# Kernel optimization log

Measured on AMD Instinct MI355X. Metric: run time of the kernel, lower is better.

Reference implementation:

```python
import jax, jax.numpy as jnp
import numpy as np

EMB = 32
B = 2048
L = 375
LAYERS = [512, 256, 128]
PROJ = 5
TABLE_SIZES = {
    'name_table': 1000001, 'collab_table': 3, 'track_uri_can_table': 1000001,
    'n_songs_table': 101, 'n_artists_table': 101, 'n_albums_table': 101,
    'artist_name_table': 300001, 'track_uri_pl_table': 1000001, 'track_name_table': 1000001,
    'duration_table': 101, 'album_name_table': 500001, 'artist_pop_table': 11,
    'followers_table': 11, 'track_pop_table': 11, 'genres_table': 2001,
}
IDX_SPECS = [
    ('name_idx', (B,), 1000001), ('collaborative_idx', (B,), 3), ('track_uri_can_idx', (B,), 1000001),
    ('n_songs_idx', (B,), 101), ('num_artists_idx', (B,), 101), ('num_albums_idx', (B,), 101),
    ('artist_name_pl_idx', (B, L), 300001), ('track_uri_pl_idx', (B, L), 1000001),
    ('track_name_pl_idx', (B, L), 1000001), ('duration_ms_idx', (B, L), 101),
    ('album_name_pl_idx', (B, L), 500001), ('artist_pop_idx', (B, L), 11),
    ('artists_followers_idx', (B, L), 11), ('track_pop_idx', (B, L), 11),
    ('artist_genres_idx', (B, L), 2001),
]


def setup_inputs() -> dict:
    key = jax.random.key(0)
    n_keys = len(IDX_SPECS) + len(TABLE_SIZES) + 10
    keys = iter(jax.random.split(key, n_keys))
    inp = {}
    for name, shape, hi in IDX_SPECS:
        inp[name] = jax.random.randint(next(keys), shape, 0, hi, dtype=jnp.int32)
    for name, n in TABLE_SIZES.items():
        inp[name] = jax.random.normal(next(keys), (n, EMB), jnp.float32) * 0.05
    d_in = 15 * EMB  # 480 concatenated features
    inp['cross_V'] = jax.random.normal(next(keys), (d_in, PROJ), jnp.float32) * 0.05
    inp['cross_U'] = jax.random.normal(next(keys), (PROJ, d_in), jnp.float32) * 0.05
    inp['cross_b'] = jnp.zeros((d_in,), jnp.float32)
    dims = [d_in] + LAYERS
    for i in range(3):
        inp[f'W{i+1}'] = jax.random.normal(next(keys), (dims[i], dims[i+1]), jnp.float32) * (1.0 / np.sqrt(dims[i]))
        inp[f'b{i+1}'] = jnp.zeros((dims[i+1],), jnp.float32)
    return inp


def _fwd(idx, tables, cross_V, cross_U, cross_b, W1, b1, W2, b2, W3, b3):
    # scalar features: single-row gather -> [B, EMB]
    # sequence features: gather [B, L, EMB] then mean-pool over L (GlobalAveragePooling1D)
    embs = []
    for ix, tab in zip(idx, tables):
        e = tab[ix]                                  # [B,EMB] or [B,L,EMB]
        if e.ndim == 3:
            e = e.mean(axis=1)                       # avg pool over playlist length
        embs.append(e)
    x0 = jnp.concatenate(embs, axis=1)               # [B, 480]
    # tfrs DCN cross layer (low-rank): x0 * ((x0 @ V) @ U + b) + x0
    proj = (x0 @ cross_V) @ cross_U + cross_b
    x = x0 * proj + x0
    # dense tower: relu, relu, linear, l2-normalize
    x = jax.nn.relu(x @ W1 + b1)
    x = jax.nn.relu(x @ W2 + b2)
    x = x @ W3 + b3
    norm = jnp.sqrt(jnp.maximum(jnp.sum(x * x, axis=1, keepdims=True), 1e-12))
    return x / norm


def reference(name_idx, collaborative_idx, track_uri_can_idx, n_songs_idx, num_artists_idx,
              num_albums_idx, artist_name_pl_idx, track_uri_pl_idx, track_name_pl_idx,
              duration_ms_idx, album_name_pl_idx, artist_pop_idx, artists_followers_idx,
              track_pop_idx, artist_genres_idx, name_table, collab_table, track_uri_can_table,
              n_songs_table, n_artists_table, n_albums_table, artist_name_table,
              track_uri_pl_table, track_name_table, duration_table, album_name_table,
              artist_pop_table, followers_table, track_pop_table, genres_table,
              cross_V, cross_U, cross_b, W1, b1, W2, b2, W3, b3):
    idx = [name_idx, collaborative_idx, track_uri_can_idx, n_songs_idx, num_artists_idx,
           num_albums_idx, artist_name_pl_idx, track_uri_pl_idx, track_name_pl_idx,
           duration_ms_idx, album_name_pl_idx, artist_pop_idx, artists_followers_idx,
           track_pop_idx, artist_genres_idx]
    tables = [name_table, collab_table, track_uri_can_table, n_songs_table, n_artists_table,
              n_albums_table, artist_name_table, track_uri_pl_table, track_name_table,
              duration_table, album_name_table, artist_pop_table, followers_table,
              track_pop_table, genres_table]
    return _fwd(idx, tables, cross_V, cross_U, cross_b, W1, b1, W2, b2, W3, b3)
```

## Files before the change

kernel.cpp:

```cpp
#include <hip/hip_runtime.h>
#include <cmath>

#define NB 2048
#define NL 375
#define NLP 384
#define NEMB 32
#define DIN 480

typedef __attribute__((ext_vector_type(8))) short short8;
typedef __attribute__((ext_vector_type(4))) short short4v;
typedef __attribute__((ext_vector_type(4))) float f32x4;

__device__ inline short f2bf(float x) {
  union { float f; unsigned u; } v; v.f = x;
  unsigned r = v.u + 0x7fffu + ((v.u >> 16) & 1u);
  return (short)(r >> 16);
}

struct SeqArgs {
  const int*   idx[9];
  const float* tab[9];
};

template <bool NT>
__device__ inline float4 gather_pool_body(const float* __restrict__ tab,
                                          const int* __restrict__ sidx,
                                          int s, int c) {
  const f32x4* tab4 = reinterpret_cast<const f32x4*>(tab);
  f32x4 acc = {0.f, 0.f, 0.f, 0.f};
  #pragma unroll
  for (int it = 0; it < 11; ++it) {
    const int l = s + it * 32;
    f32x4 v = NT ? __builtin_nontemporal_load(&tab4[(size_t)sidx[l] * 8 + c])
                 : tab4[(size_t)sidx[l] * 8 + c];
    acc += v;
  }
  {
    const int l = s + 352;
    f32x4 v = NT ? __builtin_nontemporal_load(&tab4[(size_t)sidx[l] * 8 + c])
                 : tab4[(size_t)sidx[l] * 8 + c];
    if (s < 23) acc += v;
  }
  return make_float4(acc.x, acc.y, acc.z, acc.w);
}

__global__ __launch_bounds__(256) void seq_pool_kernel(SeqArgs args, float* __restrict__ x0) {
  const int bid = blockIdx.x;
  const int f   = bid % 9;
  const int b   = bid / 9;
  const int tid = threadIdx.x;

  __shared__ int sidx[NLP];
  const int*   idx = args.idx[f];
  const float* tab = args.tab[f];

  for (int i = tid; i < NLP; i += 256)
    sidx[i] = (i < NL) ? __builtin_nontemporal_load(&idx[b * NL + i])
                       : __builtin_nontemporal_load(&idx[b * NL]);
  __syncthreads();

  const int c = tid & 7;
  const int s = tid >> 3;

  float4 acc = (f == 1 || f == 2) ? gather_pool_body<true>(tab, sidx, s, c)
                                  : gather_pool_body<false>(tab, sidx, s, c);

  #pragma unroll
  for (int off = 8; off <= 32; off <<= 1) {
    acc.x += __shfl_xor(acc.x, off, 64);
    acc.y += __shfl_xor(acc.y, off, 64);
    acc.z += __shfl_xor(acc.z, off, 64);
    acc.w += __shfl_xor(acc.w, off, 64);
  }

  __shared__ float4 wpart[4][8];
  const int wave = tid >> 6;
  const int lane = tid & 63;
  if (lane < 8) wpart[wave][lane] = acc;
  __syncthreads();

  if (tid < 8) {
    float4 s0 = wpart[0][tid], s1 = wpart[1][tid], s2 = wpart[2][tid], s3 = wpart[3][tid];
    const float inv = 1.0f / (float)NL;
    float4 r;
    r.x = (s0.x + s1.x + s2.x + s3.x) * inv;
    r.y = (s0.y + s1.y + s2.y + s3.y) * inv;
    r.z = (s0.z + s1.z + s2.z + s3.z) * inv;
    r.w = (s0.w + s1.w + s2.w + s3.w) * inv;
    float* out = x0 + (size_t)b * DIN + (6 + f) * NEMB + tid * 4;
    *reinterpret_cast<float4*>(out) = r;
  }
}

struct ScalArgs {
  const int*   idx[6];
  const float* tab[6];
};

__global__ __launch_bounds__(64) void cross_scalar_kernel(ScalArgs args,
                                                          const float* __restrict__ x0,
                                                          short* __restrict__ x0b,
                                                          const float* __restrict__ V,
                                                          const float* __restrict__ U,
                                                          const float* __restrict__ bias) {
  const int b    = blockIdx.x;
  const int lane = threadIdx.x;
  const float* row = x0 + (size_t)b * DIN;
  short* rowb = x0b + (size_t)b * DIN;

  float xv[8];
  float t[5] = {0.f, 0.f, 0.f, 0.f, 0.f};
  #pragma unroll
  for (int i = 0; i < 8; ++i) {
    int j = lane + i * 64;
    float x;
    if (i < 3) {
      int f = j >> 5, d = j & 31;
      x = args.tab[f][(size_t)args.idx[f][b] * NEMB + d];
    } else if (j < DIN) {
      x = row[j];
    } else {
      x = 0.f;
    }
    xv[i] = x;
    if (j < DIN) {
      #pragma unroll
      for (int p = 0; p < 5; ++p) t[p] += x * V[j * 5 + p];
    }
  }
  #pragma unroll
  for (int p = 0; p < 5; ++p) {
    float v = t[p];
    for (int off = 32; off; off >>= 1) v += __shfl_xor(v, off, 64);
    t[p] = v;
  }
  #pragma unroll
  for (int i = 0; i < 8; ++i) {
    int j = lane + i * 64;
    if (j < DIN) {
      float proj = bias[j];
      #pragma unroll
      for (int p = 0; p < 5; ++p) proj += t[p] * U[p * DIN + j];
      rowb[j] = f2bf(xv[i] * proj + xv[i]);
    }
  }
}

template <bool RELU>
__global__ __launch_bounds__(256) void gemm_mfma_kernel(const short* __restrict__ A,
                                                        const float* __restrict__ W,
                                                        const float* __restrict__ bias,
                                                        short* __restrict__ C,
                                                        int M, int N, int K) {
  const int tid  = threadIdx.x;
  const int m0   = blockIdx.y * 64;
  const int n0   = blockIdx.x * 64;
  const int wave = tid >> 6;
  const int lane = tid & 63;
  const int wm   = wave >> 1;
  const int wn   = wave & 1;

  __shared__ short As[64][40];
  __shared__ short Bs[64][40];

  f32x4 acc[2][2];
  #pragma unroll
  for (int i = 0; i < 2; ++i)
    #pragma unroll
    for (int j = 0; j < 2; ++j)
      acc[i][j] = (f32x4){0.f, 0.f, 0.f, 0.f};

  const int am  = tid >> 2;
  const int akq = tid & 3;
  const int bn  = tid & 63;
  const int bkg = tid >> 6;

  for (int k0 = 0; k0 < K; k0 += 32) {
    {
      short8 av = *reinterpret_cast<const short8*>(&A[(size_t)(m0 + am) * K + k0 + akq * 8]);
      *reinterpret_cast<short8*>(&As[am][akq * 8]) = av;
    }
    {
      float bv[8];
      #pragma unroll
      for (int i = 0; i < 8; ++i)
        bv[i] = W[(size_t)(k0 + bkg * 8 + i) * N + n0 + bn];
      short8 wv = { f2bf(bv[0]), f2bf(bv[1]), f2bf(bv[2]), f2bf(bv[3]),
                    f2bf(bv[4]), f2bf(bv[5]), f2bf(bv[6]), f2bf(bv[7]) };
      *reinterpret_cast<short8*>(&Bs[bn][bkg * 8]) = wv;
    }
    __syncthreads();

    short8 bf[2];
    #pragma unroll
    for (int fn = 0; fn < 2; ++fn)
      bf[fn] = *reinterpret_cast<const short8*>(&Bs[wn * 32 + fn * 16 + (lane & 15)][(lane >> 4) * 8]);
    #pragma unroll
    for (int fm = 0; fm < 2; ++fm) {
      short8 af = *reinterpret_cast<const short8*>(&As[wm * 32 + fm * 16 + (lane & 15)][(lane >> 4) * 8]);
      #pragma unroll
      for (int fn = 0; fn < 2; ++fn)
        acc[fm][fn] = __builtin_amdgcn_mfma_f32_16x16x32_bf16(af, bf[fn], acc[fm][fn], 0, 0, 0);
    }
    __syncthreads();
  }

  #pragma unroll
  for (int fm = 0; fm < 2; ++fm) {
    #pragma unroll
    for (int fn = 0; fn < 2; ++fn) {
      const int col  = n0 + wn * 32 + fn * 16 + (lane & 15);
      const float bc = bias[col];
      #pragma unroll
      for (int r = 0; r < 4; ++r) {
        const int m = m0 + wm * 32 + fm * 16 + (lane >> 4) * 4 + r;
        float x = acc[fm][fn][r] + bc;
        if (RELU) x = fmaxf(x, 0.f);
        C[(size_t)m * N + col] = f2bf(x);
      }
    }
  }
}

__global__ __launch_bounds__(256) void gemm3_norm_kernel(const short* __restrict__ A,
                                                         const float* __restrict__ W,
                                                         const float* __restrict__ bias,
                                                         float* __restrict__ out,
                                                         int M, int K) {
  const int N    = 128;
  const int tid  = threadIdx.x;
  const int m0   = blockIdx.x * 32;
  const int wave = tid >> 6;
  const int lane = tid & 63;

  __shared__ short As[32][40];
  __shared__ short Bs[128][40];

  f32x4 acc[2][2];
  #pragma unroll
  for (int i = 0; i < 2; ++i)
    #pragma unroll
    for (int j = 0; j < 2; ++j)
      acc[i][j] = (f32x4){0.f, 0.f, 0.f, 0.f};

  const int am  = tid >> 3;
  const int akq = tid & 7;
  const int bn  = tid & 127;
  const int bkg = tid >> 7;

  for (int k0 = 0; k0 < K; k0 += 32) {
    {
      short4v av = *reinterpret_cast<const short4v*>(&A[(size_t)(m0 + am) * K + k0 + akq * 4]);
      *reinterpret_cast<short4v*>(&As[am][akq * 4]) = av;
    }
    {
      float bv[16];
      #pragma unroll
      for (int i = 0; i < 16; ++i)
        bv[i] = W[(size_t)(k0 + bkg * 16 + i) * N + bn];
      short8 w0 = { f2bf(bv[0]),  f2bf(bv[1]),  f2bf(bv[2]),  f2bf(bv[3]),
                    f2bf(bv[4]),  f2bf(bv[5]),  f2bf(bv[6]),  f2bf(bv[7]) };
      short8 w1 = { f2bf(bv[8]),  f2bf(bv[9]),  f2bf(bv[10]), f2bf(bv[11]),
                    f2bf(bv[12]), f2bf(bv[13]), f2bf(bv[14]), f2bf(bv[15]) };
      *reinterpret_cast<short8*>(&Bs[bn][bkg * 16])     = w0;
      *reinterpret_cast<short8*>(&Bs[bn][bkg * 16 + 8]) = w1;
    }
    __syncthreads();

    short8 bf[2];
    #pragma unroll
    for (int fn = 0; fn < 2; ++fn)
      bf[fn] = *reinterpret_cast<const short8*>(&Bs[wave * 32 + fn * 16 + (lane & 15)][(lane >> 4) * 8]);
    #pragma unroll
    for (int fm = 0; fm < 2; ++fm) {
      short8 af = *reinterpret_cast<const short8*>(&As[fm * 16 + (lane & 15)][(lane >> 4) * 8]);
      #pragma unroll
      for (int fn = 0; fn < 2; ++fn)
        acc[fm][fn] = __builtin_amdgcn_mfma_f32_16x16x32_bf16(af, bf[fn], acc[fm][fn], 0, 0, 0);
    }
    __syncthreads();
  }

  float val[2][2][4];
  float psq[2][4] = {};
  #pragma unroll
  for (int fm = 0; fm < 2; ++fm)
    #pragma unroll
    for (int fn = 0; fn < 2; ++fn) {
      const int col  = wave * 32 + fn * 16 + (lane & 15);
      const float bc = bias[col];
      #pragma unroll
      for (int r = 0; r < 4; ++r) {
        float x = acc[fm][fn][r] + bc;
        val[fm][fn][r] = x;
        psq[fm][r] += x * x;
      }
    }

  #pragma unroll
  for (int off = 1; off < 16; off <<= 1)
    #pragma unroll
    for (int fm = 0; fm < 2; ++fm)
      #pragma unroll
      for (int r = 0; r < 4; ++r)
        psq[fm][r] += __shfl_xor(psq[fm][r], off, 64);

  __shared__ float part[4][32];
  if ((lane & 15) == 0) {
    #pragma unroll
    for (int fm = 0; fm < 2; ++fm)
      #pragma unroll
      for (int r = 0; r < 4; ++r)
        part[wave][fm * 16 + (lane >> 4) * 4 + r] = psq[fm][r];
  }
  __syncthreads();

  __shared__ float rn[32];
  if (tid < 32)
    rn[tid] = 1.0f / sqrtf(fmaxf(part[0][tid] + part[1][tid] + part[2][tid] + part[3][tid], 1e-12f));
  __syncthreads();

  #pragma unroll
  for (int fm = 0; fm < 2; ++fm)
    #pragma unroll
    for (int fn = 0; fn < 2; ++fn) {
      const int col = wave * 32 + fn * 16 + (lane & 15);
      #pragma unroll
      for (int r = 0; r < 4; ++r) {
        const int mrow = fm * 16 + (lane >> 4) * 4 + r;
        out[(size_t)(m0 + mrow) * N + col] = val[fm][fn][r] * rn[mrow];
      }
    }
}

extern "C" void kernel_launch(void* const* d_in, const int* in_sizes, int n_in,
                              void* d_out, int out_size, void* d_ws, size_t ws_size,
                              hipStream_t stream) {
  const int*   idx[15];
  const float* tab[15];
  for (int i = 0; i < 15; ++i) {
    idx[i] = (const int*)d_in[i];
    tab[i] = (const float*)d_in[15 + i];
  }
  const float* cross_V = (const float*)d_in[30];
  const float* cross_U = (const float*)d_in[31];
  const float* cross_b = (const float*)d_in[32];
  const float* W1 = (const float*)d_in[33];
  const float* b1 = (const float*)d_in[34];
  const float* W2 = (const float*)d_in[35];
  const float* b2 = (const float*)d_in[36];
  const float* W3 = (const float*)d_in[37];
  const float* b3 = (const float*)d_in[38];
  float* out = (float*)d_out;

  float* x0  = (float*)d_ws;
  short* x0b = (short*)(x0 + (size_t)NB * DIN);
  short* h1b = x0b + (size_t)NB * DIN;
  short* h2b = h1b + (size_t)NB * 512;

  SeqArgs sa;
  for (int i = 0; i < 9; ++i) { sa.idx[i] = idx[6 + i]; sa.tab[i] = tab[6 + i]; }
  ScalArgs ca;
  for (int i = 0; i < 6; ++i) { ca.idx[i] = idx[i]; ca.tab[i] = tab[i]; }

  hipLaunchKernelGGL(seq_pool_kernel, dim3(NB * 9), dim3(256), 0, stream, sa, x0);
  hipLaunchKernelGGL(cross_scalar_kernel, dim3(NB), dim3(64), 0, stream,
                     ca, x0, x0b, cross_V, cross_U, cross_b);
  hipLaunchKernelGGL((gemm_mfma_kernel<true>), dim3(512 / 64, NB / 64), dim3(256), 0, stream,
                     x0b, W1, b1, h1b, NB, 512, DIN);
  hipLaunchKernelGGL((gemm_mfma_kernel<true>), dim3(256 / 64, NB / 64), dim3(256), 0, stream,
                     h1b, W2, b2, h2b, NB, 256, 512);
  hipLaunchKernelGGL(gemm3_norm_kernel, dim3(NB / 32), dim3(256), 0, stream,
                     h2b, W3, b3, out, NB, 256);
}
```

Before: 110.2 us.

## Fuse second and third MLP GEMMs with L2-normalize into one kernel

Merges the layer-2 GEMM (512->256, ReLU) and the layer-3 GEMM plus row normalization into a single kernel. Each block handles 16 rows and keeps the intermediate h2 activations in shared memory, which removes one launch and the global write/read of h2. In exchange, every block now reloads and converts the full W2 (512x256) and W3 fp32 weights. With 128 blocks that is a lot of redundant weight traffic and conversion work per row, and there are fewer blocks to spread across CUs.

```diff
diff --git a/kernel.cpp b/kernel.cpp
--- a/kernel.cpp
+++ b/kernel.cpp
@@ -222,115 +222,138 @@
   }
 }
 
-__global__ __launch_bounds__(256) void gemm3_norm_kernel(const short* __restrict__ A,
-                                                         const float* __restrict__ W,
-                                                         const float* __restrict__ bias,
-                                                         float* __restrict__ out,
-                                                         int M, int K) {
-  const int N    = 128;
+__global__ __launch_bounds__(256) void gemm23_norm_kernel(const short* __restrict__ A,
+                                                          const float* __restrict__ W2,
+                                                          const float* __restrict__ b2,
+                                                          const float* __restrict__ W3,
+                                                          const float* __restrict__ b3,
+                                                          float* __restrict__ out) {
+  const int K1 = 512, N1 = 256, N2 = 128;
   const int tid  = threadIdx.x;
-  const int m0   = blockIdx.x * 32;
+  const int m0   = blockIdx.x * 16;
   const int wave = tid >> 6;
   const int lane = tid & 63;
 
-  __shared__ short As[32][40];
-  __shared__ short Bs[128][40];
-
-  f32x4 acc[2][2];
-  #pragma unroll
-  for (int i = 0; i < 2; ++i)
-    #pragma unroll
-    for (int j = 0; j < 2; ++j)
-      acc[i][j] = (f32x4){0.f, 0.f, 0.f, 0.f};
-
-  const int am  = tid >> 3;
-  const int akq = tid & 7;
-  const int bn  = tid & 127;
-  const int bkg = tid >> 7;
-
-  for (int k0 = 0; k0 < K; k0 += 32) {
-    {
-      short4v av = *reinterpret_cast<const short4v*>(&A[(size_t)(m0 + am) * K + k0 + akq * 4]);
-      *reinterpret_cast<short4v*>(&As[am][akq * 4]) = av;
-    }
-    {
-      float bv[16];
-      #pragma unroll
-      for (int i = 0; i < 16; ++i)
-        bv[i] = W[(size_t)(k0 + bkg * 16 + i) * N + bn];
-      short8 w0 = { f2bf(bv[0]),  f2bf(bv[1]),  f2bf(bv[2]),  f2bf(bv[3]),
-                    f2bf(bv[4]),  f2bf(bv[5]),  f2bf(bv[6]),  f2bf(bv[7]) };
-      short8 w1 = { f2bf(bv[8]),  f2bf(bv[9]),  f2bf(bv[10]), f2bf(bv[11]),
-                    f2bf(bv[12]), f2bf(bv[13]), f2bf(bv[14]), f2bf(bv[15]) };
-      *reinterpret_cast<short8*>(&Bs[bn][bkg * 16])     = w0;
-      *reinterpret_cast<short8*>(&Bs[bn][bkg * 16 + 8]) = w1;
-    }
-    __syncthreads();
-
-    short8 bf[2];
-    #pragma unroll
-    for (int fn = 0; fn < 2; ++fn)
-      bf[fn] = *reinterpret_cast<const short8*>(&Bs[wave * 32 + fn * 16 + (lane & 15)][(lane >> 4) * 8]);
-    #pragma unroll
-    for (int fm = 0; fm < 2; ++fm) {
-      short8 af = *reinterpret_cast<const short8*>(&As[fm * 16 + (lane & 15)][(lane >> 4) * 8]);
-      #pragma unroll
-      for (int fn = 0; fn < 2; ++fn)
-        acc[fm][fn] = __builtin_amdgcn_mfma_f32_16x16x32_bf16(af, bf[fn], acc[fm][fn], 0, 0, 0);
-    }
-    __syncthreads();
-  }
-
-  float val[2][2][4];
-  float psq[2][4] = {};
-  #pragma unroll
-  for (int fm = 0; fm < 2; ++fm)
+  __shared__ short As[16][40];
+  __shared__ short Bs2[256][40];
+  __shared__ short h2s[16][264];
+  __shared__ short Bs3[128][40];
+
+  f32x4 acc1[4];
+  #pragma unroll
+  for (int i = 0; i < 4; ++i) acc1[i] = (f32x4){0.f, 0.f, 0.f, 0.f};
+
+  for (int k0 = 0; k0 < K1; k0 += 32) {
+    if (tid < 64) {
+      const int row = tid >> 2, kq = tid & 3;
+      short8 av = *reinterpret_cast<const short8*>(&A[(size_t)(m0 + row) * K1 + k0 + kq * 8]);
+      *reinterpret_cast<short8*>(&As[row][kq * 8]) = av;
+    }
+    #pragma unroll
+    for (int i = 0; i < 4; ++i) {
+      const int t = i * 256 + tid;
+      const int n = t & 255, kc = t >> 8;
+      float bv[8];
+      #pragma unroll
+      for (int j = 0; j < 8; ++j)
+        bv[j] = W2[(size_t)(k0 + kc * 8 + j) * N1 + n];
+      short8 wv = { f2bf(bv[0]), f2bf(bv[1]), f2bf(bv[2]), f2bf(bv[3]),
+                    f2bf(bv[4]), f2bf(bv[5]), f2bf(bv[6]), f2bf(bv[7]) };
+      *reinterpret_cast<short8*>(&Bs2[n][kc * 8]) = wv;
+    }
+    __syncthreads();
+
+    short8 af = *reinterpret_cast<const short8*>(&As[lane & 15][(lane >> 4) * 8]);
+    #pragma unroll
+    for (int fn = 0; fn < 4; ++fn) {
+      short8 bf = *reinterpret_cast<const short8*>(&Bs2[wave * 64 + fn * 16 + (lane & 15)][(lane >> 4) * 8]);
+      acc1[fn] = __builtin_amdgcn_mfma_f32_16x16x32_bf16(af, bf, acc1[fn], 0, 0, 0);
+    }
+    __syncthreads();
+  }
+
+  #pragma unroll
+  for (int fn = 0; fn < 4; ++fn) {
+    const int col = wave * 64 + fn * 16 + (lane & 15);
+    const float bc = b2[col];
+    #pragma unroll
+    for (int r = 0; r < 4; ++r) {
+      const int row = (lane >> 4) * 4 + r;
+      h2s[row][col] = f2bf(fmaxf(acc1[fn][r] + bc, 0.f));
+    }
+  }
+  __syncthreads();
+
+  f32x4 acc2[2];
+  #pragma unroll
+  for (int i = 0; i < 2; ++i) acc2[i] = (f32x4){0.f, 0.f, 0.f, 0.f};
+
+  for (int k0 = 0; k0 < N1; k0 += 32) {
+    #pragma unroll
+    for (int i = 0; i < 2; ++i) {
+      const int t = i * 256 + tid;
+      const int n = t & 127, kc = t >> 7;
+      float bv[8];
+      #pragma unroll
+      for (int j = 0; j < 8; ++j)
+        bv[j] = W3[(size_t)(k0 + kc * 8 + j) * N2 + n];
+      short8 wv = { f2bf(bv[0]), f2bf(bv[1]), f2bf(bv[2]), f2bf(bv[3]),
+                    f2bf(bv[4]), f2bf(bv[5]), f2bf(bv[6]), f2bf(bv[7]) };
+      *reinterpret_cast<short8*>(&Bs3[n][kc * 8]) = wv;
+    }
+    __syncthreads();
+
+    short8 af = *reinterpret_cast<const short8*>(&h2s[lane & 15][k0 + (lane >> 4) * 8]);
     #pragma unroll
     for (int fn = 0; fn < 2; ++fn) {
-      const int col  = wave * 32 + fn * 16 + (lane & 15);
-      const float bc = bias[col];
-      #pragma unroll
-      for (int r = 0; r < 4; ++r) {
-        float x = acc[fm][fn][r] + bc;
-        val[fm][fn][r] = x;
-        psq[fm][r] += x * x;
-      }
-    }
+      short8 bf = *reinterpret_cast<const short8*>(&Bs3[wave * 32 + fn * 16 + (lane & 15)][(lane >> 4) * 8]);
+      acc2[fn] = __builtin_amdgcn_mfma_f32_16x16x32_bf16(af, bf, acc2[fn], 0, 0, 0);
+    }
+    __syncthreads();
+  }
+
+  float val[2][4];
+  float psq[4] = {0.f, 0.f, 0.f, 0.f};
+  #pragma unroll
+  for (int fn = 0; fn < 2; ++fn) {
+    const int col = wave * 32 + fn * 16 + (lane & 15);
+    const float bc = b3[col];
+    #pragma unroll
+    for (int r = 0; r < 4; ++r) {
+      float x = acc2[fn][r] + bc;
+      val[fn][r] = x;
+      psq[r] += x * x;
+    }
+  }
 
   #pragma unroll
   for (int off = 1; off < 16; off <<= 1)
     #pragma unroll
-    for (int fm = 0; fm < 2; ++fm)
-      #pragma unroll
-      for (int r = 0; r < 4; ++r)
-        psq[fm][r] += __shfl_xor(psq[fm][r], off, 64);
-
-  __shared__ float part[4][32];
+    for (int r = 0; r < 4; ++r)
+      psq[r] += __shfl_xor(psq[r], off, 64);
+
+  __shared__ float part[4][16];
   if ((lane & 15) == 0) {
     #pragma unroll
-    for (int fm = 0; fm < 2; ++fm)
-      #pragma unroll
-      for (int r = 0; r < 4; ++r)
-        part[wave][fm * 16 + (lane >> 4) * 4 + r] = psq[fm][r];
-  }
-  __syncthreads();
-
-  __shared__ float rn[32];
-  if (tid < 32)
+    for (int r = 0; r < 4; ++r)
+      part[wave][(lane >> 4) * 4 + r] = psq[r];
+  }
+  __syncthreads();
+
+  __shared__ float rn[16];
+  if (tid < 16)
     rn[tid] = 1.0f / sqrtf(fmaxf(part[0][tid] + part[1][tid] + part[2][tid] + part[3][tid], 1e-12f));
   __syncthreads();
 
   #pragma unroll
-  for (int fm = 0; fm < 2; ++fm)
-    #pragma unroll
-    for (int fn = 0; fn < 2; ++fn) {
-      const int col = wave * 32 + fn * 16 + (lane & 15);
-      #pragma unroll
-      for (int r = 0; r < 4; ++r) {
-        const int mrow = fm * 16 + (lane >> 4) * 4 + r;
-        out[(size_t)(m0 + mrow) * N + col] = val[fm][fn][r] * rn[mrow];
-      }
-    }
+  for (int fn = 0; fn < 2; ++fn) {
+    const int col = wave * 32 + fn * 16 + (lane & 15);
+    #pragma unroll
+    for (int r = 0; r < 4; ++r) {
+      const int row = (lane >> 4) * 4 + r;
+      out[(size_t)(m0 + row) * N2 + col] = val[fn][r] * rn[row];
+    }
+  }
 }
 
 extern "C" void kernel_launch(void* const* d_in, const int* in_sizes, int n_in,
@@ -356,7 +379,6 @@
   float* x0  = (float*)d_ws;
   short* x0b = (short*)(x0 + (size_t)NB * DIN);
   short* h1b = x0b + (size_t)NB * DIN;
-  short* h2b = h1b + (size_t)NB * 512;
 
   SeqArgs sa;
   for (int i = 0; i < 9; ++i) { sa.idx[i] = idx[6 + i]; sa.tab[i] = tab[6 + i]; }
@@ -368,8 +390,6 @@
                      ca, x0, x0b, cross_V, cross_U, cross_b);
   hipLaunchKernelGGL((gemm_mfma_kernel<true>), dim3(512 / 64, NB / 64), dim3(256), 0, stream,
                      x0b, W1, b1, h1b, NB, 512, DIN);
-  hipLaunchKernelGGL((gemm_mfma_kernel<true>), dim3(256 / 64, NB / 64), dim3(256), 0, stream,
-                     h1b, W2, b2, h2b, NB, 256, 512);
-  hipLaunchKernelGGL(gemm3_norm_kernel, dim3(NB / 32), dim3(256), 0, stream,
-                     h2b, W3, b3, out, NB, 256);
-}
+  hipLaunchKernelGGL(gemm23_norm_kernel, dim3(NB / 16), dim3(256), 0, stream,
+                     h1b, W2, b2, W3, b3, out);
+}
```

After: 112.9 us. 1.02x slower.
